# Optimization experiments

Measured on AMD Instinct MI355X. Metric: run time of the kernel, lower is better.

## Reference

```python
import jax, jax.numpy as jnp
import numpy as np

B, N, S, K = 16, 4, 64, 50        # batch, n_answers, q_len, n_boxes
VD, QD, H = 1024, 768, 512        # v_dim, q_dim, num_hid


def setup_inputs() -> dict:
    key = jax.random.key(0)
    ks = jax.random.split(key, 10)
    inp = {
        "v": jax.random.normal(ks[0], (B, 1, K, VD), dtype=jnp.float32),
        "q": jax.random.normal(ks[1], (B, N, S, 1, QD), dtype=jnp.float32),
        "box_mask": jax.random.randint(ks[2], (B, K), 0, 2, dtype=jnp.int32),
        "tags_attention": jax.random.normal(ks[3], (B, K), dtype=jnp.float32),
        # learned params (nn.Linear stores weight as [out, in])
        "Wv": jax.random.normal(ks[4], (H, VD), dtype=jnp.float32) * 0.02,
        "bv": jnp.zeros((H,), dtype=jnp.float32),
        "Wq": jax.random.normal(ks[5], (H, QD), dtype=jnp.float32) * 0.02,
        "bq": jnp.zeros((H,), dtype=jnp.float32),
        "Wl": jax.random.normal(ks[6], (1, H), dtype=jnp.float32) * 0.02,
        "bl": jnp.zeros((1,), dtype=jnp.float32),
    }
    return inp


def reference(v, q, box_mask, tags_attention, Wv, bv, Wq, bq, Wl, bl):
    # v_proj = Linear(v).unsqueeze(1): [B,1,K,H] -> [B,1,1,K,H]
    v_proj = (jnp.einsum('bokd,hd->bokh', v, Wv) + bv)[:, None]
    # q_proj: [B,N,S,1,H]
    q_proj = jnp.einsum('bnsod,hd->bnsoh', q, Wq) + bq
    # broadcast add + tanh: joint_repr [B,N,S,K,H] (the big intermediate)
    joint_repr = jnp.tanh(v_proj + q_proj)
    # score reduce over H: logits [B,N,S,K]
    logits = jnp.einsum('bnskh,oh->bnsko', joint_repr, Wl)[..., 0] + bl[0]
    # masked softmax over boxes with mask box_mask[:,None,None] -> [B,1,1,K]
    mask = (box_mask > 0)[:, None, None]
    w = jax.nn.softmax(jnp.where(mask, logits, jnp.float32(-1e9)), axis=-1)
    return w
```

## Files before the change

kernel.cpp:

```cpp
#include <hip/hip_runtime.h>
#include <hip/hip_bf16.h>
#include <cstddef>


typedef __attribute__((ext_vector_type(2))) float          f32x2;
typedef __attribute__((ext_vector_type(4))) float          f32x4;
typedef __attribute__((ext_vector_type(8))) short          bfrag;
typedef __attribute__((ext_vector_type(4))) unsigned int   u32x4;
typedef __attribute__((ext_vector_type(4))) unsigned short u16x4;

#define LGKM0  asm volatile("s_waitcnt lgkmcnt(0)" ::: "memory")
#define SBAR   __builtin_amdgcn_s_barrier()
#define SCHED0 __builtin_amdgcn_sched_barrier(0)

__device__ __forceinline__ void gload16(const void* g, void* l) {
  __builtin_amdgcn_global_load_lds((const __attribute__((address_space(1))) void*)g,
                                   (__attribute__((address_space(3))) void*)l, 16, 0, 0);
}

__device__ __forceinline__ unsigned int cvtpk(float a, float b) {
  unsigned int r;
  asm("v_cvt_pk_bf16_f32 %0, %1, %2" : "=v"(r) : "v"(a), "v"(b));
  return r;
}

__device__ __forceinline__ float bf2f(unsigned short u) {
  return __uint_as_float((unsigned int)u << 16);
}

template<int CTRL>
__device__ __forceinline__ float dpp_add(float x) {
  int r = __builtin_amdgcn_update_dpp(0, __float_as_int(x), CTRL, 0xF, 0xF, false);
  return x + __int_as_float(r);
}

__global__ void __launch_bounds__(256) gemm_fused(
    const float* __restrict__ v,  const float* __restrict__ q,
    const float* __restrict__ Wv, const float* __restrict__ bv,
    const float* __restrict__ Wq, const float* __restrict__ bq,
    unsigned short* __restrict__ evw, float* __restrict__ qpw) {
  __shared__ unsigned short As[2][64 * 64];
  __shared__ unsigned short Bs[2][64 * 64];

  const int id = blockIdx.x;
  const int m  = (id & 7) + ((id >> 6) << 3);
  const int nt = (id >> 3) & 7;
  if (m >= 77) return;

  const int t = threadIdx.x;

  const float* A; const float* W; const float* bias;
  int M, Kd, m0;
  const bool vpath = (m < 13);
  if (vpath) { A = v; W = Wv; bias = bv; M = 800;  Kd = 1024; m0 = m * 64; }
  else       { A = q; W = Wq; bias = bq; M = 4096; Kd = 768;  m0 = (m - 13) * 64; }
  const int n0 = nt * 64;

  const int lane = t & 63;
  const int wave = t >> 6;
  const int wm   = wave >> 1;
  const int wn   = wave & 1;
  const int la   = lane & 15;
  const int lb   = lane >> 4;

  const int srow = t >> 2;
  const int skq  = (t & 3) * 16;

  int gr = m0 + srow; if (gr >= M) gr = M - 1;
  const float* Arow = A + (size_t)gr * Kd + skq;
  const float* Wrow = W + (size_t)(n0 + srow) * Kd + skq;

  f32x4 acc[2][2] = {};
  f32x4 raA[4], rbA[4], raB[4], rbB[4];

  auto loadG = [&](f32x4* ra, f32x4* rb, int s) {
    const float* ap = Arow + s * 64;
    const float* wp = Wrow + s * 64;
#pragma unroll
    for (int i = 0; i < 4; ++i) ra[i] = *(const f32x4*)&ap[i * 4];
#pragma unroll
    for (int i = 0; i < 4; ++i) rb[i] = *(const f32x4*)&wp[i * 4];
  };

  const int o0 = (srow * 128 + skq * 2)      ^ ((srow & 7) << 4);
  const int o1 = (srow * 128 + skq * 2 + 16) ^ ((srow & 7) << 4);

  auto writeL = [&](unsigned short* da, unsigned short* db,
                    const f32x4* ra, const f32x4* rb) {
    u32x4 p;
    p[0] = cvtpk(ra[0][0], ra[0][1]); p[1] = cvtpk(ra[0][2], ra[0][3]);
    p[2] = cvtpk(ra[1][0], ra[1][1]); p[3] = cvtpk(ra[1][2], ra[1][3]);
    *(u32x4*)((char*)da + o0) = p;
    p[0] = cvtpk(ra[2][0], ra[2][1]); p[1] = cvtpk(ra[2][2], ra[2][3]);
    p[2] = cvtpk(ra[3][0], ra[3][1]); p[3] = cvtpk(ra[3][2], ra[3][3]);
    *(u32x4*)((char*)da + o1) = p;
    p[0] = cvtpk(rb[0][0], rb[0][1]); p[1] = cvtpk(rb[0][2], rb[0][3]);
    p[2] = cvtpk(rb[1][0], rb[1][1]); p[3] = cvtpk(rb[1][2], rb[1][3]);
    *(u32x4*)((char*)db + o0) = p;
    p[0] = cvtpk(rb[2][0], rb[2][1]); p[1] = cvtpk(rb[2][2], rb[2][3]);
    p[2] = cvtpk(rb[3][0], rb[3][1]); p[3] = cvtpk(rb[3][2], rb[3][3]);
    *(u32x4*)((char*)db + o1) = p;
  };

  auto compute = [&](const unsigned short* sa, const unsigned short* sb) {
    bfrag af[2][2], bf[2][2];
#pragma unroll
    for (int r = 0; r < 2; ++r)
#pragma unroll
      for (int kk = 0; kk < 2; ++kk) {
        int rowa = wm * 32 + r * 16 + la;
        af[r][kk] = *(const bfrag*)((const char*)sa +
                     ((rowa * 128 + kk * 64 + lb * 16) ^ ((rowa & 7) << 4)));
        int rowb = wn * 32 + r * 16 + la;
        bf[r][kk] = *(const bfrag*)((const char*)sb +
                     ((rowb * 128 + kk * 64 + lb * 16) ^ ((rowb & 7) << 4)));
      }
#pragma unroll
    for (int kk = 0; kk < 2; ++kk)
#pragma unroll
      for (int r = 0; r < 2; ++r)
#pragma unroll
        for (int c = 0; c < 2; ++c)
          acc[r][c] = __builtin_amdgcn_mfma_f32_16x16x32_bf16(af[r][kk], bf[c][kk], acc[r][c], 0, 0, 0);
  };

  const int nsteps = Kd >> 6;
  loadG(raA, rbA, 0);
  writeL(As[0], Bs[0], raA, rbA);
  loadG(raA, rbA, 1);
  loadG(raB, rbB, 2);
  LGKM0; SCHED0; SBAR; SCHED0;
  for (int s = 0; s < nsteps; s += 2) {
    compute(As[0], Bs[0]);
    SBAR; SCHED0;
    writeL(As[1], Bs[1], raA, rbA);
    if (s + 3 < nsteps) loadG(raA, rbA, s + 3);
    LGKM0; SCHED0; SBAR; SCHED0;
    compute(As[1], Bs[1]);
    SBAR; SCHED0;
    if (s + 2 < nsteps) {
      writeL(As[0], Bs[0], raB, rbB);
      if (s + 4 < nsteps) loadG(raB, rbB, s + 4);
      LGKM0; SCHED0;
    }
    SBAR; SCHED0;
  }

  const float CEXP = 2.885390081777927f;
#pragma unroll
  for (int c = 0; c < 2; ++c) {
    int col = n0 + wn * 32 + c * 16 + la;
    float bcol = bias[col];
#pragma unroll
    for (int r = 0; r < 2; ++r) {
      int mbase = m0 + wm * 32 + r * 16 + lb * 4;
#pragma unroll
      for (int e = 0; e < 4; ++e) {
        int mr = mbase + e;
        if (mr < M) {
          float val = __builtin_amdgcn_exp2f((acc[r][c][e] + bcol) * CEXP);
          if (vpath) evw[(size_t)mr * 512 + col] = (unsigned short)cvtpk(val, val);
          else       qpw[(size_t)mr * 512 + col] = val;
        }
      }
    }
  }
}

__global__ void
__attribute__((amdgpu_flat_work_group_size(512, 512), amdgpu_waves_per_eu(4, 4)))
stage3_kernel(
    const unsigned short* __restrict__ ev, const float* __restrict__ qp,
    const float* __restrict__ wl, const int* __restrict__ box_mask,
    float* __restrict__ out) {
  __shared__ unsigned short vpS[50][512];
  __shared__ float redS[8][64][8];

  const int b    = blockIdx.y;
  const int grp  = blockIdx.x;
  const int t    = threadIdx.x;
  const int wv   = t >> 6;
  const int lane = t & 63;
  const int row0 = b * 256 + grp * 16 + wv * 2;

  const float* q0 = qp + (size_t)row0 * 512;
  float eq0[8], eq1[8], wlr[8];
#pragma unroll
  for (int j = 0; j < 2; ++j) {
    f32x4 a = *(const f32x4*)&q0[j * 256 + 4 * lane];
    f32x4 c = *(const f32x4*)&q0[512 + j * 256 + 4 * lane];
    f32x4 w = *(const f32x4*)&wl[j * 256 + 4 * lane];
#pragma unroll
    for (int e = 0; e < 4; ++e) {
      eq0[j * 4 + e] = a[e];
      eq1[j * 4 + e] = c[e];
      wlr[j * 4 + e] = -2.f * w[e];
    }
  }

  {
    const unsigned short* src = ev + (size_t)b * 25600 + lane * 8;
#pragma unroll
    for (int i = 0; i < 7; ++i) {
      int kr = i * 8 + wv;
      if (kr < 50) gload16(src + kr * 512, &vpS[kr][0]);
    }
  }
  __syncthreads();

  const int g  = lane >> 4;
  const int li = lane & 15;

#pragma unroll 1
  for (int kc = 0; kc < 5; ++kc) {
    float a0[10], a1[10];
#pragma unroll
    for (int i = 0; i < 10; ++i) { a0[i] = 0.f; a1[i] = 0.f; }

#pragma unroll
    for (int i = 0; i < 10; ++i) {
      const unsigned short* vr = &vpS[kc * 10 + i][0];
      u16x4 va = *(const u16x4*)&vr[4 * lane];
      u16x4 vb = *(const u16x4*)&vr[256 + 4 * lane];
#pragma unroll
      for (int e = 0; e < 4; ++e) {
        float evf = bf2f(va[e]);
        a0[i] = fmaf(wlr[e], __builtin_amdgcn_rcpf(fmaf(evf, eq0[e], 1.f)), a0[i]);
        a1[i] = fmaf(wlr[e], __builtin_amdgcn_rcpf(fmaf(evf, eq1[e], 1.f)), a1[i]);
      }
#pragma unroll
      for (int e = 0; e < 4; ++e) {
        float evf = bf2f(vb[e]);
        a0[i] = fmaf(wlr[4 + e], __builtin_amdgcn_rcpf(fmaf(evf, eq0[4 + e], 1.f)), a0[i]);
        a1[i] = fmaf(wlr[4 + e], __builtin_amdgcn_rcpf(fmaf(evf, eq1[4 + e], 1.f)), a1[i]);
      }
    }

#pragma unroll
    for (int i = 0; i < 10; ++i) {
      int k = kc * 10 + i;
      float s0 = a0[i], s1 = a1[i];
      s0 = dpp_add<0x128>(s0); s0 = dpp_add<0x124>(s0);
      s0 = dpp_add<0x122>(s0); s0 = dpp_add<0x121>(s0);
      s1 = dpp_add<0x128>(s1); s1 = dpp_add<0x124>(s1);
      s1 = dpp_add<0x122>(s1); s1 = dpp_add<0x121>(s1);
      if (li == (k & 15)) {
        f32x2 p; p[0] = s0; p[1] = s1;
        *(f32x2*)&redS[wv][k][g * 2] = p;
      }
    }
  }

  const int k = lane;
  f32x4 ra = *(const f32x4*)&redS[wv][k][0];
  f32x4 rb = *(const f32x4*)&redS[wv][k][4];
  float l0 = (ra[0] + ra[2]) + (rb[0] + rb[2]);
  float l1 = (ra[1] + ra[3]) + (rb[1] + rb[3]);

  int   msk = (k < 50) ? box_mask[b * 50 + k] : 0;
  bool  on  = (k < 50 && msk > 0);
  float L0 = on ? l0 : -1e9f;
  float L1 = on ? l1 : -1e9f;

  float m0 = L0, m1 = L1;
#pragma unroll
  for (int off = 32; off; off >>= 1) {
    m0 = fmaxf(m0, __shfl_xor(m0, off));
    m1 = fmaxf(m1, __shfl_xor(m1, off));
  }
  const float LOG2E = 1.4426950408889634f;
  float e0 = (k < 50) ? __builtin_amdgcn_exp2f((L0 - m0) * LOG2E) : 0.f;
  float e1 = (k < 50) ? __builtin_amdgcn_exp2f((L1 - m1) * LOG2E) : 0.f;
  float s0 = e0, s1 = e1;
#pragma unroll
  for (int off = 32; off; off >>= 1) {
    s0 += __shfl_xor(s0, off);
    s1 += __shfl_xor(s1, off);
  }

  if (k < 50) {
    out[(size_t)row0 * 50 + k]       = e0 / s0;
    out[(size_t)(row0 + 1) * 50 + k] = e1 / s1;
  }
}

extern "C" void kernel_launch(void* const* d_in, const int* in_sizes, int n_in,
                              void* d_out, int out_size, void* d_ws, size_t ws_size,
                              hipStream_t stream) {
  const float* v        = (const float*)d_in[0];
  const float* q        = (const float*)d_in[1];
  const int*   box_mask = (const int*)d_in[2];
  const float* Wv       = (const float*)d_in[4];
  const float* bv       = (const float*)d_in[5];
  const float* Wq       = (const float*)d_in[6];
  const float* bq       = (const float*)d_in[7];
  const float* Wl       = (const float*)d_in[8];
  float* out = (float*)d_out;

  char* ws = (char*)d_ws;
  float*          qpw = (float*)(ws);
  unsigned short* evw = (unsigned short*)(ws + 8388608);

  gemm_fused<<<dim3(640),     256, 0, stream>>>(v, q, Wv, bv, Wq, bq, evw, qpw);
  stage3_kernel<<<dim3(16, 16), 512, 0, stream>>>(evw, qpw, Wl, box_mask, out);
}
```

Baseline: 49.33 us.

## Pre-convert inputs to bf16 and stream GEMM tiles directly into LDS

Adds a separate kernel that converts v, q, Wv and Wq from fp32 to bf16 in workspace buffers. The GEMM then loads bf16 tiles with global_load_lds straight into swizzled, double-buffered LDS, waiting on vmcnt instead of staging through registers. This is meant to halve GEMM global traffic and remove per-tile register conversion and LDS writes. In exchange it adds an extra kernel launch and a full read and write pass over all inputs every call.

```diff
diff --git a/kernel.cpp b/kernel.cpp
--- a/kernel.cpp
+++ b/kernel.cpp
@@ -6,10 +6,9 @@
 typedef __attribute__((ext_vector_type(2))) float          f32x2;
 typedef __attribute__((ext_vector_type(4))) float          f32x4;
 typedef __attribute__((ext_vector_type(8))) short          bfrag;
-typedef __attribute__((ext_vector_type(4))) unsigned int   u32x4;
+typedef __attribute__((ext_vector_type(2))) unsigned int   u32x2;
 typedef __attribute__((ext_vector_type(4))) unsigned short u16x4;
 
-#define LGKM0  asm volatile("s_waitcnt lgkmcnt(0)" ::: "memory")
 #define SBAR   __builtin_amdgcn_s_barrier()
 #define SCHED0 __builtin_amdgcn_sched_barrier(0)
 
@@ -34,10 +33,28 @@
   return x + __int_as_float(r);
 }
 
-__global__ void __launch_bounds__(256) gemm_fused(
-    const float* __restrict__ v,  const float* __restrict__ q,
-    const float* __restrict__ Wv, const float* __restrict__ bv,
-    const float* __restrict__ Wq, const float* __restrict__ bq,
+__global__ void __launch_bounds__(256) cvt_all(
+    const float* __restrict__ v, const float* __restrict__ wv,
+    const float* __restrict__ q, const float* __restrict__ wq,
+    unsigned short* __restrict__ vb, unsigned short* __restrict__ wvb,
+    unsigned short* __restrict__ qb, unsigned short* __restrict__ wqb) {
+  const int total = 1220608;
+  for (int f = blockIdx.x * 256 + threadIdx.x; f < total; f += gridDim.x * 256) {
+    const float* src; unsigned short* dst; int off;
+    if (f < 204800)       { src = v;  dst = vb;  off = f; }
+    else if (f < 335872)  { src = wv; dst = wvb; off = f - 204800; }
+    else if (f < 1122304) { src = q;  dst = qb;  off = f - 335872; }
+    else                  { src = wq; dst = wqb; off = f - 1122304; }
+    f32x4 x = ((const f32x4*)src)[off];
+    u32x2 p; p[0] = cvtpk(x[0], x[1]); p[1] = cvtpk(x[2], x[3]);
+    ((u32x2*)dst)[off] = p;
+  }
+}
+
+__global__ void __launch_bounds__(256) gemm_bf16(
+    const unsigned short* __restrict__ vb, const unsigned short* __restrict__ qb,
+    const unsigned short* __restrict__ wvb, const unsigned short* __restrict__ wqb,
+    const float* __restrict__ bv, const float* __restrict__ bq,
     unsigned short* __restrict__ evw, float* __restrict__ qpw) {
   __shared__ unsigned short As[2][64 * 64];
   __shared__ unsigned short Bs[2][64 * 64];
@@ -49,11 +66,11 @@
 
   const int t = threadIdx.x;
 
-  const float* A; const float* W; const float* bias;
+  const unsigned short* A; const unsigned short* W; const float* bias;
   int M, Kd, m0;
   const bool vpath = (m < 13);
-  if (vpath) { A = v; W = Wv; bias = bv; M = 800;  Kd = 1024; m0 = m * 64; }
-  else       { A = q; W = Wq; bias = bq; M = 4096; Kd = 768;  m0 = (m - 13) * 64; }
+  if (vpath) { A = vb; W = wvb; bias = bv; M = 800;  Kd = 1024; m0 = m * 64; }
+  else       { A = qb; W = wqb; bias = bq; M = 4096; Kd = 768;  m0 = (m - 13) * 64; }
   const int n0 = nt * 64;
 
   const int lane = t & 63;
@@ -63,44 +80,27 @@
   const int la   = lane & 15;
   const int lb   = lane >> 4;
 
-  const int srow = t >> 2;
-  const int skq  = (t & 3) * 16;
-
-  int gr = m0 + srow; if (gr >= M) gr = M - 1;
-  const float* Arow = A + (size_t)gr * Kd + skq;
-  const float* Wrow = W + (size_t)(n0 + srow) * Kd + skq;
+  const int row1 = t >> 3;
+  const int p1   = (t & 7) ^ (row1 & 7);
+  int grA1 = m0 + row1;      if (grA1 >= M) grA1 = M - 1;
+  int grA2 = m0 + row1 + 32; if (grA2 >= M) grA2 = M - 1;
+  const unsigned short* srcA1 = A + (size_t)grA1 * Kd + p1 * 8;
+  const unsigned short* srcA2 = A + (size_t)grA2 * Kd + p1 * 8;
+  const unsigned short* srcB1 = W + (size_t)(n0 + row1) * Kd + p1 * 8;
+  const unsigned short* srcB2 = W + (size_t)(n0 + row1 + 32) * Kd + p1 * 8;
+
+  const int d1 = wave * 512;
+  const int d2 = 2048 + wave * 512;
+
+  auto STAGE = [&](int buf, int s) {
+    const int o = s * 64;
+    gload16(srcA1 + o, &As[buf][d1]);
+    gload16(srcA2 + o, &As[buf][d2]);
+    gload16(srcB1 + o, &Bs[buf][d1]);
+    gload16(srcB2 + o, &Bs[buf][d2]);
+  };
 
   f32x4 acc[2][2] = {};
-  f32x4 raA[4], rbA[4], raB[4], rbB[4];
-
-  auto loadG = [&](f32x4* ra, f32x4* rb, int s) {
-    const float* ap = Arow + s * 64;
-    const float* wp = Wrow + s * 64;
-#pragma unroll
-    for (int i = 0; i < 4; ++i) ra[i] = *(const f32x4*)&ap[i * 4];
-#pragma unroll
-    for (int i = 0; i < 4; ++i) rb[i] = *(const f32x4*)&wp[i * 4];
-  };
-
-  const int o0 = (srow * 128 + skq * 2)      ^ ((srow & 7) << 4);
-  const int o1 = (srow * 128 + skq * 2 + 16) ^ ((srow & 7) << 4);
-
-  auto writeL = [&](unsigned short* da, unsigned short* db,
-                    const f32x4* ra, const f32x4* rb) {
-    u32x4 p;
-    p[0] = cvtpk(ra[0][0], ra[0][1]); p[1] = cvtpk(ra[0][2], ra[0][3]);
-    p[2] = cvtpk(ra[1][0], ra[1][1]); p[3] = cvtpk(ra[1][2], ra[1][3]);
-    *(u32x4*)((char*)da + o0) = p;
-    p[0] = cvtpk(ra[2][0], ra[2][1]); p[1] = cvtpk(ra[2][2], ra[2][3]);
-    p[2] = cvtpk(ra[3][0], ra[3][1]); p[3] = cvtpk(ra[3][2], ra[3][3]);
-    *(u32x4*)((char*)da + o1) = p;
-    p[0] = cvtpk(rb[0][0], rb[0][1]); p[1] = cvtpk(rb[0][2], rb[0][3]);
-    p[2] = cvtpk(rb[1][0], rb[1][1]); p[3] = cvtpk(rb[1][2], rb[1][3]);
-    *(u32x4*)((char*)db + o0) = p;
-    p[0] = cvtpk(rb[2][0], rb[2][1]); p[1] = cvtpk(rb[2][2], rb[2][3]);
-    p[2] = cvtpk(rb[3][0], rb[3][1]); p[3] = cvtpk(rb[3][2], rb[3][3]);
-    *(u32x4*)((char*)db + o1) = p;
-  };
 
   auto compute = [&](const unsigned short* sa, const unsigned short* sb) {
     bfrag af[2][2], bf[2][2];
@@ -125,25 +125,16 @@
   };
 
   const int nsteps = Kd >> 6;
-  loadG(raA, rbA, 0);
-  writeL(As[0], Bs[0], raA, rbA);
-  loadG(raA, rbA, 1);
-  loadG(raB, rbB, 2);
-  LGKM0; SCHED0; SBAR; SCHED0;
-  for (int s = 0; s < nsteps; s += 2) {
-    compute(As[0], Bs[0]);
+  STAGE(0, 0);
+  STAGE(1, 1);
+  for (int s = 0; s < nsteps; ++s) {
+    if (s + 1 < nsteps) { asm volatile("s_waitcnt vmcnt(4)" ::: "memory"); }
+    else                { asm volatile("s_waitcnt vmcnt(0)" ::: "memory"); }
+    SCHED0;
     SBAR; SCHED0;
-    writeL(As[1], Bs[1], raA, rbA);
-    if (s + 3 < nsteps) loadG(raA, rbA, s + 3);
-    LGKM0; SCHED0; SBAR; SCHED0;
-    compute(As[1], Bs[1]);
+    compute(As[s & 1], Bs[s & 1]);
     SBAR; SCHED0;
-    if (s + 2 < nsteps) {
-      writeL(As[0], Bs[0], raB, rbB);
-      if (s + 4 < nsteps) loadG(raB, rbB, s + 4);
-      LGKM0; SCHED0;
-    }
-    SBAR; SCHED0;
+    if (s + 2 < nsteps) STAGE(s & 1, s + 2);
   }
 
   const float CEXP = 2.885390081777927f;
@@ -221,7 +212,7 @@
     for (int i = 0; i < 10; ++i) {
       const unsigned short* vr = &vpS[kc * 10 + i][0];
       u16x4 va = *(const u16x4*)&vr[4 * lane];
-      u16x4 vb = *(const u16x4*)&vr[256 + 4 * lane];
+      u16x4 vb2 = *(const u16x4*)&vr[256 + 4 * lane];
 #pragma unroll
       for (int e = 0; e < 4; ++e) {
         float evf = bf2f(va[e]);
@@ -230,7 +221,7 @@
       }
 #pragma unroll
       for (int e = 0; e < 4; ++e) {
-        float evf = bf2f(vb[e]);
+        float evf = bf2f(vb2[e]);
         a0[i] = fmaf(wlr[4 + e], __builtin_amdgcn_rcpf(fmaf(evf, eq0[4 + e], 1.f)), a0[i]);
         a1[i] = fmaf(wlr[4 + e], __builtin_amdgcn_rcpf(fmaf(evf, eq1[4 + e], 1.f)), a1[i]);
       }
@@ -300,7 +291,12 @@
   char* ws = (char*)d_ws;
   float*          qpw = (float*)(ws);
   unsigned short* evw = (unsigned short*)(ws + 8388608);
-
-  gemm_fused<<<dim3(640),     256, 0, stream>>>(v, q, Wv, bv, Wq, bq, evw, qpw);
+  unsigned short* vb  = (unsigned short*)(ws + 9207808);
+  unsigned short* qb  = (unsigned short*)(ws + 10846208);
+  unsigned short* wvb = (unsigned short*)(ws + 17137664);
+  unsigned short* wqb = (unsigned short*)(ws + 18186240);
+
+  cvt_all<<<2048, 256, 0, stream>>>(v, Wv, q, Wq, vb, wvb, qb, wqb);
+  gemm_bf16<<<dim3(640), 256, 0, stream>>>(vb, qb, wvb, wqb, bv, bq, evw, qpw);
   stage3_kernel<<<dim3(16, 16), 512, 0, stream>>>(evw, qpw, Wl, box_mask, out);
 }
```

After: 45.87 us. 1.08x faster.
